# Kernel optimization log

Hardware: AMD Instinct MI355X
Metric: run time of the kernel (lower is better)

The kernel has to match this reference:

```python
import jax, jax.numpy as jnp
import numpy as np

N = 50000   # nodes per node type
D = 128     # in/out channels
E = 500000  # edges per edge type


def setup_inputs() -> dict:
    key = jax.random.key(0)
    ks = jax.random.split(key, 24)
    s = 1.0 / np.sqrt(D)
    def w(k, shape):
        return jax.random.normal(k, shape, jnp.float32) * s
    inp = {
        "x_a": jax.random.normal(ks[0], (N, D), jnp.float32),
        "x_b": jax.random.normal(ks[1], (N, D), jnp.float32),
        "edge_e1": jax.random.randint(ks[2], (2, E), 0, N),  # a -> b
        "edge_e2": jax.random.randint(ks[3], (2, E), 0, N),  # b -> a
        "edge_e3": jax.random.randint(ks[4], (2, E), 0, N),  # b -> a
    }
    i = 5
    for e in ("e1", "e2", "e3"):
        inp[f"Ws_{e}"] = w(ks[i], (D, D)); i += 1
        inp[f"Wt_{e}"] = w(ks[i], (D, D)); i += 1
        inp[f"wih_{e}"] = w(ks[i], (3 * D, D)); i += 1
        inp[f"whh_{e}"] = w(ks[i], (3 * D, D)); i += 1
        inp[f"bih_{e}"] = jnp.zeros((3 * D,), jnp.float32)
        inp[f"bhh_{e}"] = jnp.zeros((3 * D,), jnp.float32)
    return inp


def _gru_cell(x, h, wih, whh, bih, bhh):
    # PyTorch nn.GRUCell semantics: x = input, h = hidden
    gi = x @ wih.T + bih
    gh = h @ whh.T + bhh
    ir, iz, inn = jnp.split(gi, 3, axis=1)
    hr, hz, hn = jnp.split(gh, 3, axis=1)
    r = jax.nn.sigmoid(ir + hr)
    z = jax.nn.sigmoid(iz + hz)
    n = jnp.tanh(inn + r * hn)
    return (1.0 - z) * n + z * h


def _edge_type(x_src, x_tgt, edge, Ws, Wt, wih, whh, bih, bhh):
    sx = x_src @ Ws.T                       # [Ns, D] per-edge-type source linear (no bias)
    tx = x_tgt @ Wt.T                       # [Nt, D] per-edge-type target linear
    msg = sx[edge[0]]                       # [E, D]  gather by source index
    agg = jax.ops.segment_sum(msg, edge[1], num_segments=x_tgt.shape[0])  # scatter-sum
    return _gru_cell(tx, agg, wih, whh, bih, bhh)


def reference(x_a, x_b, edge_e1, edge_e2, edge_e3,
              Ws_e1, Wt_e1, wih_e1, whh_e1, bih_e1, bhh_e1,
              Ws_e2, Wt_e2, wih_e2, whh_e2, bih_e2, bhh_e2,
              Ws_e3, Wt_e3, wih_e3, whh_e3, bih_e3, bhh_e3):
    # edge type e1: a -> b  (div['b'] = 1)
    out_b = _edge_type(x_a, x_b, edge_e1, Ws_e1, Wt_e1, wih_e1, whh_e1, bih_e1, bhh_e1)
    # edge types e2, e3: b -> a  (div['a'] = 2)
    out_a = _edge_type(x_b, x_a, edge_e2, Ws_e2, Wt_e2, wih_e2, whh_e2, bih_e2, bhh_e2)
    out_a = out_a + _edge_type(x_b, x_a, edge_e3, Ws_e3, Wt_e3, wih_e3, whh_e3, bih_e3, bhh_e3)
    out_a = out_a / 2.0
    out_a = jax.nn.relu(out_a)
    out_b = jax.nn.relu(out_b)
    return jnp.stack([out_a, out_b])  # [2, N, D]
```

## Files before the change

kernel.cpp:

```cpp
#include <hip/hip_runtime.h>
#include <hip/hip_bf16.h>
#include <stdint.h>
#include <math.h>

#define NN 50000
#define DD 128
#define EE 500000
#define ROWT 1563
#define NBIN 98

typedef __attribute__((ext_vector_type(8))) short bfx8;
typedef __attribute__((ext_vector_type(4))) short bfx4;
typedef __attribute__((ext_vector_type(4))) float f32x4;
typedef __attribute__((ext_vector_type(4))) int i32x4;
typedef unsigned short u16;

static __device__ __forceinline__ short f2bf(float f) {
  union { float f; uint32_t u; } v; v.f = f;
  uint32_t r = (v.u + 0x7fffu + ((v.u >> 16) & 1u)) >> 16;
  return (short)r;
}
static __device__ __forceinline__ float bf2f(short b) {
  union { uint32_t u; float f; } v; v.u = ((uint32_t)(uint16_t)b) << 16;
  return v.f;
}

static __device__ __forceinline__ void gl_lds16(const short* g, short* l) {
  __builtin_amdgcn_global_load_lds(
      (const __attribute__((address_space(1))) unsigned int*)g,
      (__attribute__((address_space(3))) unsigned int*)l, 16, 0, 0);
}

static __device__ __forceinline__ bfx8 load_pk(const short* p, int ct, int ks, int lane) {
  return *reinterpret_cast<const bfx8*>(p + ((((size_t)ct * 4 + ks) * 64 + lane) << 3));
}

struct PrepArgs {
  const float* csrc[2]; short* cdst[2];
  const float* A[6]; const float* B[6]; short* pout[6];
  const float* psrc[3]; short* pdst[3];
};

__global__ __launch_bounds__(256) void k_prep(PrepArgs p) {
  const int y = blockIdx.y;
  if (y < 2) {
    int i = (blockIdx.x * 256 + threadIdx.x) * 4;
    if (i >= NN * DD) return;
    f32x4 v = *reinterpret_cast<const f32x4*>(p.csrc[y] + i);
    bfx4 o;
    o[0]=f2bf(v[0]); o[1]=f2bf(v[1]); o[2]=f2bf(v[2]); o[3]=f2bf(v[3]);
    *reinterpret_cast<bfx4*>(p.cdst[y] + i) = o;
  } else if (y < 8) {
    if (blockIdx.x >= 192) return;
    const int e = y - 2;
    const float* A = p.A[e];
    const float* B = p.B[e];
    int tid = blockIdx.x * 256 + threadIdx.x;
    int i = tid >> 7, j = tid & 127;
    float acc = 0.f;
    #pragma unroll 4
    for (int k = 0; k < 128; ++k) acc += A[i * 128 + k] * B[k * 128 + j];
    int ct = i >> 4;
    int lane = (i & 15) | ((((j & 31) >> 3)) << 4);
    int ks = j >> 5;
    int elem = j & 7;
    p.pout[e][(((size_t)(ct * 4 + ks) * 64 + lane) << 3) + elem] = f2bf(acc);
  } else {
    if (blockIdx.x >= 8) return;
    const int jb = y - 8;
    int tid = blockIdx.x * 256 + threadIdx.x;
    int lane = tid & 63, ks = (tid >> 6) & 3, ct = tid >> 8;
    const float* s = p.psrc[jb] + (size_t)(ct * 16 + (lane & 15)) * 128 + ks * 32 + ((lane >> 4) << 3);
    bfx8 o;
    #pragma unroll
    for (int i = 0; i < 8; ++i) o[i] = f2bf(s[i]);
    *reinterpret_cast<bfx8*>(p.pdst[jb] + ((size_t)tid << 3)) = o;
  }
}

struct CsrArgs {
  const int* edge[3];
  int* ccnt;
  int* cstart;
  int* ccur;
  uint32_t* cbkt[3];
  int* offs[3];
  u16* bucket[3];
};

__global__ __launch_bounds__(256) void k_chist(CsrArgs a) {
  const int t = blockIdx.y, tid = threadIdx.x;
  __shared__ int cnt[NBIN];
  for (int b = tid; b < NBIN; b += 256) cnt[b] = 0;
  __syncthreads();
  const int* ed = a.edge[t];
  int base = blockIdx.x * 2048;
  #pragma unroll
  for (int m = 0; m < 8; ++m) {
    int i = base + m * 256 + tid;
    if (i < EE) atomicAdd(&cnt[ed[EE + i] >> 9], 1);
  }
  __syncthreads();
  for (int b = tid; b < NBIN; b += 256)
    if (cnt[b]) atomicAdd(&a.ccnt[t * NBIN + b], cnt[b]);
}

__global__ __launch_bounds__(384) void k_cscan(CsrArgs a) {
  __shared__ int buf[3][128];
  int ty = threadIdx.x >> 7;
  int i = threadIdx.x & 127;
  int v = (i < NBIN) ? a.ccnt[ty * NBIN + i] : 0;
  buf[ty][i] = v;
  __syncthreads();
  for (int off = 1; off < 128; off <<= 1) {
    int tv = (i >= off) ? buf[ty][i - off] : 0;
    __syncthreads();
    buf[ty][i] += tv;
    __syncthreads();
  }
  if (i < NBIN) {
    int excl = buf[ty][i] - v;
    a.cstart[ty * NBIN + i] = excl;
    a.ccur[ty * NBIN + i] = excl;
  }
}

__global__ __launch_bounds__(256) void k_cbin(CsrArgs a) {
  const int t = blockIdx.y, tid = threadIdx.x;
  __shared__ int cnt[NBIN], cur[NBIN];
  for (int b = tid; b < NBIN; b += 256) cnt[b] = 0;
  __syncthreads();
  const int* ed = a.edge[t];
  int base = blockIdx.x * 4096;
  #pragma unroll
  for (int m = 0; m < 16; ++m) {
    int i = base + m * 256 + tid;
    if (i < EE) atomicAdd(&cnt[ed[EE + i] >> 9], 1);
  }
  __syncthreads();
  for (int b = tid; b < NBIN; b += 256)
    cur[b] = cnt[b] ? atomicAdd(&a.ccur[t * NBIN + b], cnt[b]) : 0;
  __syncthreads();
  uint32_t* cb = a.cbkt[t];
  #pragma unroll
  for (int m = 0; m < 16; ++m) {
    int i = base + m * 256 + tid;
    if (i < EE) {
      int tg = ed[EE + i];
      int b = tg >> 9;
      int pos = atomicAdd(&cur[b], 1);
      cb[pos] = (uint32_t)ed[i] | ((uint32_t)(tg & 511) << 20);
    }
  }
}

__global__ __launch_bounds__(256) void k_fsort(CsrArgs a) {
  const int t = blockIdx.y, bin = blockIdx.x, tid = threadIdx.x;
  __shared__ int rc[512], rcur[512], sb[256];
  int s0 = a.cstart[t * NBIN + bin];
  int cntb = a.ccnt[t * NBIN + bin];
  rc[tid] = 0; rc[tid + 256] = 0;
  __syncthreads();
  const uint32_t* cb = a.cbkt[t];
  for (int i = tid; i < cntb; i += 256) atomicAdd(&rc[cb[s0 + i] >> 20], 1);
  __syncthreads();
  int A = rc[2 * tid], B = rc[2 * tid + 1], s = A + B;
  sb[tid] = s;
  __syncthreads();
  for (int off = 1; off < 256; off <<= 1) {
    int v = (tid >= off) ? sb[tid - off] : 0;
    __syncthreads();
    sb[tid] += v;
    __syncthreads();
  }
  int excl = sb[tid] - s;
  rcur[2 * tid] = s0 + excl;
  rcur[2 * tid + 1] = s0 + excl + A;
  int rows0 = bin << 9;
  int nr = NN - rows0; if (nr > 512) nr = 512;
  if (2 * tid < nr)     a.offs[t][rows0 + 2 * tid]     = s0 + excl + A;
  if (2 * tid + 1 < nr) a.offs[t][rows0 + 2 * tid + 1] = s0 + excl + A + B;
  __syncthreads();
  u16* fb = a.bucket[t];
  for (int i = tid; i < cntb; i += 256) {
    uint32_t e = cb[s0 + i];
    int pos = atomicAdd(&rcur[e >> 20], 1);
    fb[pos] = (u16)e;
  }
}

struct GArgs {
  const int* offs[3]; const u16* bkt[3];
  const short* xsrc[3]; short* agg[3];
};

__global__ __launch_bounds__(256) void k_gather(GArgs a) {
  const int ty = blockIdx.y;
  const int* __restrict__ offs = a.offs[ty];
  const u16* __restrict__ bucket = a.bkt[ty];
  const short* __restrict__ xsrc = a.xsrc[ty];
  short* __restrict__ agg = a.agg[ty];
  int tid = threadIdx.x;
  int row = blockIdx.x * 32 + (tid >> 3);
  if (row >= NN) return;
  int c0 = (tid & 7) * 16;
  int start = row ? offs[row - 1] : 0;
  int end = offs[row];
  f32x4 s0 = (f32x4)(0.f), s1 = (f32x4)(0.f), s2 = (f32x4)(0.f), s3 = (f32x4)(0.f);
  int i = start;
  for (; i + 8 <= end; i += 8) {
    const short* pp[8];
    #pragma unroll
    for (int m = 0; m < 8; ++m) pp[m] = xsrc + (size_t)bucket[i + m] * DD + c0;
    #pragma unroll
    for (int m = 0; m < 8; ++m) {
      bfx8 u = *reinterpret_cast<const bfx8*>(pp[m]);
      bfx8 v = *reinterpret_cast<const bfx8*>(pp[m] + 8);
      #pragma unroll
      for (int j = 0; j < 4; ++j) {
        s0[j] += bf2f(u[j]); s1[j] += bf2f(u[4+j]);
        s2[j] += bf2f(v[j]); s3[j] += bf2f(v[4+j]);
      }
    }
  }
  for (; i + 4 <= end; i += 4) {
    const short* pp[4];
    #pragma unroll
    for (int m = 0; m < 4; ++m) pp[m] = xsrc + (size_t)bucket[i + m] * DD + c0;
    #pragma unroll
    for (int m = 0; m < 4; ++m) {
      bfx8 u = *reinterpret_cast<const bfx8*>(pp[m]);
      bfx8 v = *reinterpret_cast<const bfx8*>(pp[m] + 8);
      #pragma unroll
      for (int j = 0; j < 4; ++j) {
        s0[j] += bf2f(u[j]); s1[j] += bf2f(u[4+j]);
        s2[j] += bf2f(v[j]); s3[j] += bf2f(v[4+j]);
      }
    }
  }
  for (; i < end; ++i) {
    const short* p = xsrc + (size_t)bucket[i] * DD + c0;
    bfx8 u = *reinterpret_cast<const bfx8*>(p), v = *reinterpret_cast<const bfx8*>(p + 8);
    #pragma unroll
    for (int j = 0; j < 4; ++j) {
      s0[j] += bf2f(u[j]); s1[j] += bf2f(u[4+j]);
      s2[j] += bf2f(v[j]); s3[j] += bf2f(v[4+j]);
    }
  }
  short* d = agg + (size_t)row * DD + c0;
  bfx8 o0, o1;
  #pragma unroll
  for (int j = 0; j < 4; ++j) {
    o0[j] = f2bf(s0[j]); o0[4+j] = f2bf(s1[j]);
    o1[j] = f2bf(s2[j]); o1[4+j] = f2bf(s3[j]);
  }
  *reinterpret_cast<bfx8*>(d) = o0;
  *reinterpret_cast<bfx8*>(d + 8) = o1;
}

static __device__ __forceinline__ void gru8(const f32x4 h[2], const f32x4 ai[2][3],
                                            const f32x4 ah[2][3],
                                            float bir, float biz, float bin,
                                            float bhr, float bhz, float bhn,
                                            f32x4 res[2]) {
  #pragma unroll
  for (int rf = 0; rf < 2; ++rf)
    #pragma unroll
    for (int q = 0; q < 4; ++q) {
      float ir = ai[rf][0][q] + bir, iz = ai[rf][1][q] + biz, in = ai[rf][2][q] + bin;
      float hr = ah[rf][0][q] + bhr, hz = ah[rf][1][q] + bhz, hn = ah[rf][2][q] + bhn;
      float rr = 1.f / (1.f + __expf(-(ir + hr)));
      float zz = 1.f / (1.f + __expf(-(iz + hz)));
      float t2 = in + rr * hn;
      float nn = 1.f - 2.f / (__expf(2.f * t2) + 1.f);
      res[rf][q] = (1.f - zz) * nn + zz * h[rf][q];
    }
}

static __device__ __forceinline__ void gru_unit(
    const short* lds, int gbase, int ctw, int lane,
    const short* wsp, const short* combp, const short* whhsp,
    f32x4 (&h)[2], f32x4 (&ai)[2][3], f32x4 (&ah)[2][3]) {
  #pragma unroll
  for (int rf = 0; rf < 2; ++rf) {
    h[rf] = (f32x4)(0.f);
    #pragma unroll
    for (int g = 0; g < 3; ++g) { ai[rf][g] = (f32x4)(0.f); ah[rf][g] = (f32x4)(0.f); }
  }
  #pragma unroll
  for (int ks = 0; ks < 4; ++ks) {
    bfx8 x0 = *reinterpret_cast<const bfx8*>(lds + (0 + ks) * 512 + lane * 8);
    bfx8 x1 = *reinterpret_cast<const bfx8*>(lds + (4 + ks) * 512 + lane * 8);
    bfx8 g0 = *reinterpret_cast<const bfx8*>(lds + (gbase + ks) * 512 + lane * 8);
    bfx8 g1 = *reinterpret_cast<const bfx8*>(lds + (gbase + 4 + ks) * 512 + lane * 8);
    bfx8 bws = load_pk(wsp, ctw, ks, lane);
    h[0] = __builtin_amdgcn_mfma_f32_16x16x32_bf16(g0, bws, h[0], 0, 0, 0);
    h[1] = __builtin_amdgcn_mfma_f32_16x16x32_bf16(g1, bws, h[1], 0, 0, 0);
    #pragma unroll
    for (int g = 0; g < 3; ++g) {
      int ct = g * 8 + ctw;
      bfx8 bi = load_pk(combp, ct, ks, lane);
      bfx8 bh = load_pk(whhsp, ct, ks, lane);
      ai[0][g] = __builtin_amdgcn_mfma_f32_16x16x32_bf16(x0, bi, ai[0][g], 0, 0, 0);
      ai[1][g] = __builtin_amdgcn_mfma_f32_16x16x32_bf16(x1, bi, ai[1][g], 0, 0, 0);
      ah[0][g] = __builtin_amdgcn_mfma_f32_16x16x32_bf16(g0, bh, ah[0][g], 0, 0, 0);
      ah[1][g] = __builtin_amdgcn_mfma_f32_16x16x32_bf16(g1, bh, ah[1][g], 0, 0, 0);
    }
  }
}

struct GG1Args {
  const short* aggX; const short* xt;
  const short* wsp; const short* combp; const short* whhsp;
  const float* bih; const float* bhh;
  float* out;
};

__global__ __launch_bounds__(512) void k_ggru1(GG1Args a) {
  __shared__ short lds[16 * 512];
  const int wave = threadIdx.x >> 6, lane = threadIdx.x & 63;
  const int rbase = blockIdx.x * 32;
  const int ctw = wave;

  #pragma unroll
  for (int i = 0; i < 2; ++i) {
    int f = wave * 2 + i;
    const short* src = (f & 8) ? a.aggX : a.xt;
    int r = rbase + ((f >> 2) & 1) * 16 + (lane & 15);
    if (r >= NN) r = NN - 1;
    gl_lds16(src + (size_t)r * DD + (f & 3) * 32 + ((lane >> 4) << 3), lds + f * 512);
  }
  __syncthreads();

  f32x4 h[2], ai[2][3], ah[2][3];
  gru_unit(lds, 8, ctw, lane, a.wsp, a.combp, a.whhsp, h, ai, ah);

  const int col = ctw * 16 + (lane & 15);
  f32x4 res[2];
  gru8(h, ai, ah, a.bih[col], a.bih[128 + col], a.bih[256 + col],
       a.bhh[col], a.bhh[128 + col], a.bhh[256 + col], res);
  const int lq = (lane >> 4) << 2;
  #pragma unroll
  for (int rf = 0; rf < 2; ++rf)
    #pragma unroll
    for (int q = 0; q < 4; ++q) {
      int r = rbase + rf * 16 + lq + q;
      if (r < NN) a.out[(size_t)r * DD + col] = fmaxf(res[rf][q], 0.f);
    }
}

struct GG2Args {
  const short* agg2; const short* agg3; const short* xt;
  const short* wsp2; const short* combp2; const short* whhsp2;
  const short* wsp3; const short* combp3; const short* whhsp3;
  const float* bih2; const float* bhh2;
  const float* bih3; const float* bhh3;
  float* out;
};

__global__ __launch_bounds__(512) void k_ggru2(GG2Args a) {
  __shared__ short lds[24 * 512];
  __shared__ float r3buf[32 * 68];
  const int wave = threadIdx.x >> 6, lane = threadIdx.x & 63;
  const int rbase = (blockIdx.x >> 1) * 32;
  const int colblk = blockIdx.x & 1;
  const int unit = wave >> 2;
  const int ctw = colblk * 4 + (wave & 3);

  #pragma unroll
  for (int i = 0; i < 3; ++i) {
    int f = wave * 3 + i;
    const short* src = (f < 8) ? a.xt : ((f < 16) ? a.agg2 : a.agg3);
    int r = rbase + ((f >> 2) & 1) * 16 + (lane & 15);
    if (r >= NN) r = NN - 1;
    gl_lds16(src + (size_t)r * DD + (f & 3) * 32 + ((lane >> 4) << 3), lds + f * 512);
  }
  __syncthreads();

  const short* wspU   = unit ? a.wsp3   : a.wsp2;
  const short* combpU = unit ? a.combp3 : a.combp2;
  const short* whhspU = unit ? a.whhsp3 : a.whhsp2;
  const float* bihU   = unit ? a.bih3   : a.bih2;
  const float* bhhU   = unit ? a.bhh3   : a.bhh2;
  const int gbase = unit ? 16 : 8;

  f32x4 h[2], ai[2][3], ah[2][3];
  gru_unit(lds, gbase, ctw, lane, wspU, combpU, whhspU, h, ai, ah);

  const int col = ctw * 16 + (lane & 15);
  const int cl = (wave & 3) * 16 + (lane & 15);
  const int lq = (lane >> 4) << 2;
  f32x4 res[2];
  gru8(h, ai, ah, bihU[col], bihU[128 + col], bihU[256 + col],
       bhhU[col], bhhU[128 + col], bhhU[256 + col], res);

  if (unit == 1) {
    #pragma unroll
    for (int rf = 0; rf < 2; ++rf)
      #pragma unroll
      for (int q = 0; q < 4; ++q)
        r3buf[(rf * 16 + lq + q) * 68 + cl] = res[rf][q];
  }
  __syncthreads();
  if (unit == 0) {
    #pragma unroll
    for (int rf = 0; rf < 2; ++rf)
      #pragma unroll
      for (int q = 0; q < 4; ++q) {
        int r = rbase + rf * 16 + lq + q;
        if (r < NN) {
          float r3 = r3buf[(rf * 16 + lq + q) * 68 + cl];
          a.out[(size_t)r * DD + col] = fmaxf((res[rf][q] + r3) * 0.5f, 0.f);
        }
      }
  }
}

extern "C" void kernel_launch(void* const* d_in, const int* in_sizes, int n_in,
                              void* d_out, int out_size, void* d_ws, size_t ws_size,
                              hipStream_t stream) {
  const float* x_a = (const float*)d_in[0];
  const float* x_b = (const float*)d_in[1];
  const int* edges[3] = {(const int*)d_in[2], (const int*)d_in[3], (const int*)d_in[4]};
  const float *Ws[3], *Wt[3], *wih[3], *whh[3], *bih[3], *bhh[3];
  for (int e = 0; e < 3; ++e) {
    int b = 5 + e * 6;
    Ws[e]  = (const float*)d_in[b + 0];
    Wt[e]  = (const float*)d_in[b + 1];
    wih[e] = (const float*)d_in[b + 2];
    whh[e] = (const float*)d_in[b + 3];
    bih[e] = (const float*)d_in[b + 4];
    bhh[e] = (const float*)d_in[b + 5];
  }

  char* ws = (char*)d_ws;
  short* xa_bf  = (short*)ws;
  short* xb_bf  = (short*)(ws + 12800000);
  short* aggX   = (short*)(ws + 25600000);
  int*   offs   = (int*)(ws + 64000000);
  u16*   bucket = (u16*)(ws + 64600000);
  uint32_t* cbkt= (uint32_t*)(ws + 67600000);
  short* pk     = (short*)(ws + 73600000);
  int*   ccnt   = (int*)(ws + 74300000);
  int*   cstart = (int*)(ws + 74310000);
  int*   ccur   = (int*)(ws + 74320000);
  short *wsp[3], *combp[3], *whhsp[3];
  short* aggp[3];
  int* offsp[3]; u16* bktp[3]; uint32_t* cbktp[3];
  for (int e = 0; e < 3; ++e) {
    short* base = pk + (size_t)e * 114688;
    wsp[e] = base; combp[e] = base + 16384; whhsp[e] = base + 65536;
    aggp[e]  = aggX + (size_t)e * NN * DD;
    offsp[e] = offs + (size_t)e * 50000;
    bktp[e]  = bucket + (size_t)e * 500000;
    cbktp[e] = cbkt + (size_t)e * 500000;
  }

  PrepArgs pa;
  pa.csrc[0] = x_a; pa.cdst[0] = xa_bf;
  pa.csrc[1] = x_b; pa.cdst[1] = xb_bf;
  for (int e = 0; e < 3; ++e) {
    pa.A[e] = wih[e];     pa.B[e] = Wt[e]; pa.pout[e] = combp[e];
    pa.A[3 + e] = whh[e]; pa.B[3 + e] = Ws[e]; pa.pout[3 + e] = whhsp[e];
    pa.psrc[e] = Ws[e];   pa.pdst[e] = wsp[e];
  }
  hipLaunchKernelGGL(k_prep, dim3(6250, 11), dim3(256), 0, stream, pa);

  CsrArgs ca;
  for (int e = 0; e < 3; ++e) {
    ca.edge[e] = edges[e];
    ca.cbkt[e] = cbktp[e];
    ca.offs[e] = offsp[e];
    ca.bucket[e] = bktp[e];
  }
  ca.ccnt = ccnt; ca.cstart = cstart; ca.ccur = ccur;
  (void)hipMemsetAsync(ccnt, 0, 3 * NBIN * sizeof(int), stream);
  hipLaunchKernelGGL(k_chist, dim3((EE + 2047) / 2048, 3), dim3(256), 0, stream, ca);
  hipLaunchKernelGGL(k_cscan, dim3(1), dim3(384), 0, stream, ca);
  hipLaunchKernelGGL(k_cbin, dim3((EE + 4095) / 4096, 3), dim3(256), 0, stream, ca);
  hipLaunchKernelGGL(k_fsort, dim3(NBIN, 3), dim3(256), 0, stream, ca);

  GArgs ga;
  const short* srcb[3] = {xa_bf, xb_bf, xb_bf};
  for (int e = 0; e < 3; ++e) {
    ga.offs[e] = offsp[e]; ga.bkt[e] = bktp[e];
    ga.xsrc[e] = srcb[e];  ga.agg[e] = aggp[e];
  }
  hipLaunchKernelGGL(k_gather, dim3(ROWT, 3), dim3(256), 0, stream, ga);

  float* out_a = (float*)d_out;
  float* out_b = (float*)d_out + (size_t)NN * DD;

  GG1Args g1 = {aggp[0], xb_bf, wsp[0], combp[0], whhsp[0], bih[0], bhh[0], out_b};
  hipLaunchKernelGGL(k_ggru1, dim3(ROWT), dim3(512), 0, stream, g1);

  GG2Args g2 = {aggp[1], aggp[2], xa_bf,
                wsp[1], combp[1], whhsp[1],
                wsp[2], combp[2], whhsp[2],
                bih[1], bhh[1], bih[2], bhh[2], out_a};
  hipLaunchKernelGGL(k_ggru2, dim3(ROWT * 2), dim3(512), 0, stream, g2);
}
```

Measured before the change: 227.4 us.

## Fuse GRU kernels into one launch with double-buffered row tiles; fold histogram into prep

Merges the two GRU-update kernels into a single launch where each block handles two row tiles, prefetching the second tile into LDS while computing the first. It also folds the edge-destination histogram into the prep kernel as extra grid rows, removing a separate launch. The aim is to cut launch overhead and hide the global-to-LDS load latency. In exchange LDS use per block doubles, which may lower occupancy, and r3buf now aliases the first tile's buffer, which needs the added barriers to stay correct.

```diff
diff --git a/kernel.cpp b/kernel.cpp
--- a/kernel.cpp
+++ b/kernel.cpp
@@ -8,6 +8,9 @@
 #define EE 500000
 #define ROWT 1563
 #define NBIN 98
+#define GG2GRID 1564
+#define GG1GRID 782
+#define CHB 245
 
 typedef __attribute__((ext_vector_type(8))) short bfx8;
 typedef __attribute__((ext_vector_type(4))) short bfx4;
@@ -39,6 +42,7 @@
   const float* csrc[2]; short* cdst[2];
   const float* A[6]; const float* B[6]; short* pout[6];
   const float* psrc[3]; short* pdst[3];
+  const int* edge[3]; int* ccnt;
 };
 
 __global__ __launch_bounds__(256) void k_prep(PrepArgs p) {
@@ -65,7 +69,7 @@
     int ks = j >> 5;
     int elem = j & 7;
     p.pout[e][(((size_t)(ct * 4 + ks) * 64 + lane) << 3) + elem] = f2bf(acc);
-  } else {
+  } else if (y < 11) {
     if (blockIdx.x >= 8) return;
     const int jb = y - 8;
     int tid = blockIdx.x * 256 + threadIdx.x;
@@ -75,6 +79,22 @@
     #pragma unroll
     for (int i = 0; i < 8; ++i) o[i] = f2bf(s[i]);
     *reinterpret_cast<bfx8*>(p.pdst[jb] + ((size_t)tid << 3)) = o;
+  } else {
+    if (blockIdx.x >= CHB) return;
+    const int t = y - 11, tid = threadIdx.x;
+    __shared__ int cnt[NBIN];
+    for (int b = tid; b < NBIN; b += 256) cnt[b] = 0;
+    __syncthreads();
+    const int* ed = p.edge[t];
+    int base = blockIdx.x * 2048;
+    #pragma unroll
+    for (int m = 0; m < 8; ++m) {
+      int i = base + m * 256 + tid;
+      if (i < EE) atomicAdd(&cnt[ed[EE + i] >> 9], 1);
+    }
+    __syncthreads();
+    for (int b = tid; b < NBIN; b += 256)
+      if (cnt[b]) atomicAdd(&p.ccnt[t * NBIN + b], cnt[b]);
   }
 }
 
@@ -87,23 +107,6 @@
   int* offs[3];
   u16* bucket[3];
 };
-
-__global__ __launch_bounds__(256) void k_chist(CsrArgs a) {
-  const int t = blockIdx.y, tid = threadIdx.x;
-  __shared__ int cnt[NBIN];
-  for (int b = tid; b < NBIN; b += 256) cnt[b] = 0;
-  __syncthreads();
-  const int* ed = a.edge[t];
-  int base = blockIdx.x * 2048;
-  #pragma unroll
-  for (int m = 0; m < 8; ++m) {
-    int i = base + m * 256 + tid;
-    if (i < EE) atomicAdd(&cnt[ed[EE + i] >> 9], 1);
-  }
-  __syncthreads();
-  for (int b = tid; b < NBIN; b += 256)
-    if (cnt[b]) atomicAdd(&a.ccnt[t * NBIN + b], cnt[b]);
-}
 
 __global__ __launch_bounds__(384) void k_cscan(CsrArgs a) {
   __shared__ int buf[3][128];
@@ -309,91 +312,36 @@
   }
 }
 
-struct GG1Args {
-  const short* aggX; const short* xt;
-  const short* wsp; const short* combp; const short* whhsp;
-  const float* bih; const float* bhh;
-  float* out;
-};
-
-__global__ __launch_bounds__(512) void k_ggru1(GG1Args a) {
-  __shared__ short lds[16 * 512];
-  const int wave = threadIdx.x >> 6, lane = threadIdx.x & 63;
-  const int rbase = blockIdx.x * 32;
-  const int ctw = wave;
-
-  #pragma unroll
-  for (int i = 0; i < 2; ++i) {
-    int f = wave * 2 + i;
-    const short* src = (f & 8) ? a.aggX : a.xt;
-    int r = rbase + ((f >> 2) & 1) * 16 + (lane & 15);
-    if (r >= NN) r = NN - 1;
-    gl_lds16(src + (size_t)r * DD + (f & 3) * 32 + ((lane >> 4) << 3), lds + f * 512);
-  }
-  __syncthreads();
-
-  f32x4 h[2], ai[2][3], ah[2][3];
-  gru_unit(lds, 8, ctw, lane, a.wsp, a.combp, a.whhsp, h, ai, ah);
-
-  const int col = ctw * 16 + (lane & 15);
-  f32x4 res[2];
-  gru8(h, ai, ah, a.bih[col], a.bih[128 + col], a.bih[256 + col],
-       a.bhh[col], a.bhh[128 + col], a.bhh[256 + col], res);
-  const int lq = (lane >> 4) << 2;
-  #pragma unroll
-  for (int rf = 0; rf < 2; ++rf)
-    #pragma unroll
-    for (int q = 0; q < 4; ++q) {
-      int r = rbase + rf * 16 + lq + q;
-      if (r < NN) a.out[(size_t)r * DD + col] = fmaxf(res[rf][q], 0.f);
-    }
-}
-
-struct GG2Args {
-  const short* agg2; const short* agg3; const short* xt;
+struct GGArgs {
+  const short* xa; const short* xb;
+  const short* agg1; const short* agg2; const short* agg3;
+  const short* wsp1; const short* combp1; const short* whhsp1;
   const short* wsp2; const short* combp2; const short* whhsp2;
   const short* wsp3; const short* combp3; const short* whhsp3;
+  const float* bih1; const float* bhh1;
   const float* bih2; const float* bhh2;
   const float* bih3; const float* bhh3;
-  float* out;
+  float* out_a; float* out_b;
 };
 
-__global__ __launch_bounds__(512) void k_ggru2(GG2Args a) {
-  __shared__ short lds[24 * 512];
-  __shared__ float r3buf[32 * 68];
-  const int wave = threadIdx.x >> 6, lane = threadIdx.x & 63;
-  const int rbase = (blockIdx.x >> 1) * 32;
-  const int colblk = blockIdx.x & 1;
+static __device__ __forceinline__ void tile2(const short* buf, float* r3buf, const GGArgs& a,
+                                             int rbase, int colblk, int wave, int lane) {
   const int unit = wave >> 2;
   const int ctw = colblk * 4 + (wave & 3);
-
-  #pragma unroll
-  for (int i = 0; i < 3; ++i) {
-    int f = wave * 3 + i;
-    const short* src = (f < 8) ? a.xt : ((f < 16) ? a.agg2 : a.agg3);
-    int r = rbase + ((f >> 2) & 1) * 16 + (lane & 15);
-    if (r >= NN) r = NN - 1;
-    gl_lds16(src + (size_t)r * DD + (f & 3) * 32 + ((lane >> 4) << 3), lds + f * 512);
-  }
-  __syncthreads();
-
   const short* wspU   = unit ? a.wsp3   : a.wsp2;
   const short* combpU = unit ? a.combp3 : a.combp2;
   const short* whhspU = unit ? a.whhsp3 : a.whhsp2;
   const float* bihU   = unit ? a.bih3   : a.bih2;
   const float* bhhU   = unit ? a.bhh3   : a.bhh2;
-  const int gbase = unit ? 16 : 8;
-
   f32x4 h[2], ai[2][3], ah[2][3];
-  gru_unit(lds, gbase, ctw, lane, wspU, combpU, whhspU, h, ai, ah);
-
+  gru_unit(buf, unit ? 16 : 8, ctw, lane, wspU, combpU, whhspU, h, ai, ah);
   const int col = ctw * 16 + (lane & 15);
   const int cl = (wave & 3) * 16 + (lane & 15);
   const int lq = (lane >> 4) << 2;
   f32x4 res[2];
   gru8(h, ai, ah, bihU[col], bihU[128 + col], bihU[256 + col],
        bhhU[col], bhhU[128 + col], bhhU[256 + col], res);
-
+  __syncthreads();
   if (unit == 1) {
     #pragma unroll
     for (int rf = 0; rf < 2; ++rf)
@@ -410,9 +358,85 @@
         int r = rbase + rf * 16 + lq + q;
         if (r < NN) {
           float r3 = r3buf[(rf * 16 + lq + q) * 68 + cl];
-          a.out[(size_t)r * DD + col] = fmaxf((res[rf][q] + r3) * 0.5f, 0.f);
+          a.out_a[(size_t)r * DD + col] = fmaxf((res[rf][q] + r3) * 0.5f, 0.f);
         }
       }
+  }
+}
+
+static __device__ __forceinline__ void tile1(const short* buf, const GGArgs& a,
+                                             int rbase, int wave, int lane) {
+  const int ctw = wave;
+  f32x4 h[2], ai[2][3], ah[2][3];
+  gru_unit(buf, 8, ctw, lane, a.wsp1, a.combp1, a.whhsp1, h, ai, ah);
+  const int col = ctw * 16 + (lane & 15);
+  f32x4 res[2];
+  gru8(h, ai, ah, a.bih1[col], a.bih1[128 + col], a.bih1[256 + col],
+       a.bhh1[col], a.bhh1[128 + col], a.bhh1[256 + col], res);
+  const int lq = (lane >> 4) << 2;
+  #pragma unroll
+  for (int rf = 0; rf < 2; ++rf)
+    #pragma unroll
+    for (int q = 0; q < 4; ++q) {
+      int r = rbase + rf * 16 + lq + q;
+      if (r < NN) a.out_b[(size_t)r * DD + col] = fmaxf(res[rf][q], 0.f);
+    }
+}
+
+__global__ __launch_bounds__(512) void k_ggru(GGArgs a) {
+  __shared__ short lds[2 * 24 * 512];
+  float* r3buf = (float*)lds;
+  const int wave = threadIdx.x >> 6, lane = threadIdx.x & 63;
+  const int bx = blockIdx.x;
+  if (bx < GG2GRID) {
+    const int pair = bx >> 1, colblk = bx & 1;
+    const int rt1 = pair * 2 + 1;
+    const int rb0 = (pair * 2) * 32;
+    const int rb1 = (rt1 < ROWT ? rt1 : pair * 2) * 32;
+    #pragma unroll
+    for (int i = 0; i < 3; ++i) {
+      int f = wave * 3 + i;
+      const short* src = (f < 8) ? a.xa : ((f < 16) ? a.agg2 : a.agg3);
+      int r = rb0 + ((f >> 2) & 1) * 16 + (lane & 15);
+      if (r >= NN) r = NN - 1;
+      gl_lds16(src + (size_t)r * DD + (f & 3) * 32 + ((lane >> 4) << 3), lds + f * 512);
+    }
+    __syncthreads();
+    #pragma unroll
+    for (int i = 0; i < 3; ++i) {
+      int f = wave * 3 + i;
+      const short* src = (f < 8) ? a.xa : ((f < 16) ? a.agg2 : a.agg3);
+      int r = rb1 + ((f >> 2) & 1) * 16 + (lane & 15);
+      if (r >= NN) r = NN - 1;
+      gl_lds16(src + (size_t)r * DD + (f & 3) * 32 + ((lane >> 4) << 3), lds + (24 + f) * 512);
+    }
+    tile2(lds, r3buf, a, rb0, colblk, wave, lane);
+    if (rt1 < ROWT) tile2(lds + 24 * 512, r3buf, a, rb1, colblk, wave, lane);
+  } else {
+    const int bxg = bx - GG2GRID;
+    const int rt1 = bxg * 2 + 1;
+    const int rb0 = (bxg * 2) * 32;
+    const int rb1 = (rt1 < ROWT ? rt1 : bxg * 2) * 32;
+    #pragma unroll
+    for (int i = 0; i < 2; ++i) {
+      int f = wave * 2 + i;
+      const short* src = (f & 8) ? a.agg1 : a.xb;
+      int r = rb0 + ((f >> 2) & 1) * 16 + (lane & 15);
+      if (r >= NN) r = NN - 1;
+      gl_lds16(src + (size_t)r * DD + (f & 3) * 32 + ((lane >> 4) << 3), lds + f * 512);
+    }
+    __syncthreads();
+    #pragma unroll
+    for (int i = 0; i < 2; ++i) {
+      int f = wave * 2 + i;
+      const short* src = (f & 8) ? a.agg1 : a.xb;
+      int r = rb1 + ((f >> 2) & 1) * 16 + (lane & 15);
+      if (r >= NN) r = NN - 1;
+      gl_lds16(src + (size_t)r * DD + (f & 3) * 32 + ((lane >> 4) << 3), lds + (24 + f) * 512);
+    }
+    tile1(lds, a, rb0, wave, lane);
+    __syncthreads();
+    if (rt1 < ROWT) tile1(lds + 24 * 512, a, rb1, wave, lane);
   }
 }
 
@@ -456,6 +480,8 @@
     cbktp[e] = cbkt + (size_t)e * 500000;
   }
 
+  (void)hipMemsetAsync(ccnt, 0, 3 * NBIN * sizeof(int), stream);
+
   PrepArgs pa;
   pa.csrc[0] = x_a; pa.cdst[0] = xa_bf;
   pa.csrc[1] = x_b; pa.cdst[1] = xb_bf;
@@ -463,8 +489,10 @@
     pa.A[e] = wih[e];     pa.B[e] = Wt[e]; pa.pout[e] = combp[e];
     pa.A[3 + e] = whh[e]; pa.B[3 + e] = Ws[e]; pa.pout[3 + e] = whhsp[e];
     pa.psrc[e] = Ws[e];   pa.pdst[e] = wsp[e];
-  }
-  hipLaunchKernelGGL(k_prep, dim3(6250, 11), dim3(256), 0, stream, pa);
+    pa.edge[e] = edges[e];
+  }
+  pa.ccnt = ccnt;
+  hipLaunchKernelGGL(k_prep, dim3(6250, 14), dim3(256), 0, stream, pa);
 
   CsrArgs ca;
   for (int e = 0; e < 3; ++e) {
@@ -474,8 +502,6 @@
     ca.bucket[e] = bktp[e];
   }
   ca.ccnt = ccnt; ca.cstart = cstart; ca.ccur = ccur;
-  (void)hipMemsetAsync(ccnt, 0, 3 * NBIN * sizeof(int), stream);
-  hipLaunchKernelGGL(k_chist, dim3((EE + 2047) / 2048, 3), dim3(256), 0, stream, ca);
   hipLaunchKernelGGL(k_cscan, dim3(1), dim3(384), 0, stream, ca);
   hipLaunchKernelGGL(k_cbin, dim3((EE + 4095) / 4096, 3), dim3(256), 0, stream, ca);
   hipLaunchKernelGGL(k_fsort, dim3(NBIN, 3), dim3(256), 0, stream, ca);
@@ -491,12 +517,15 @@
   float* out_a = (float*)d_out;
   float* out_b = (float*)d_out + (size_t)NN * DD;
 
-  GG1Args g1 = {aggp[0], xb_bf, wsp[0], combp[0], whhsp[0], bih[0], bhh[0], out_b};
-  hipLaunchKernelGGL(k_ggru1, dim3(ROWT), dim3(512), 0, stream, g1);
-
-  GG2Args g2 = {aggp[1], aggp[2], xa_bf,
-                wsp[1], combp[1], whhsp[1],
-                wsp[2], combp[2], whhsp[2],
-                bih[1], bhh[1], bih[2], bhh[2], out_a};
-  hipLaunchKernelGGL(k_ggru2, dim3(ROWT * 2), dim3(512), 0, stream, g2);
-}
+  GGArgs gg;
+  gg.xa = xa_bf; gg.xb = xb_bf;
+  gg.agg1 = aggp[0]; gg.agg2 = aggp[1]; gg.agg3 = aggp[2];
+  gg.wsp1 = wsp[0]; gg.combp1 = combp[0]; gg.whhsp1 = whhsp[0];
+  gg.wsp2 = wsp[1]; gg.combp2 = combp[1]; gg.whhsp2 = whhsp[1];
+  gg.wsp3 = wsp[2]; gg.combp3 = combp[2]; gg.whhsp3 = whhsp[2];
+  gg.bih1 = bih[0]; gg.bhh1 = bhh[0];
+  gg.bih2 = bih[1]; gg.bhh2 = bhh[1];
+  gg.bih3 = bih[2]; gg.bhh3 = bhh[2];
+  gg.out_a = out_a; gg.out_b = out_b;
+  hipLaunchKernelGGL(k_ggru, dim3(GG2GRID + GG1GRID), dim3(512), 0, stream, gg);
+}
```

New measurement: 246.5 us. +8.4%, slower.
